# Performance work log

Measured on AMD Instinct MI355X. Metric: run time of the kernel, lower is better.

Reference implementation:

```python
import jax, jax.numpy as jnp
import numpy as np

BS, SL, D_IN, D_MODEL, H = 4, 128, 512, 512, 8
DP = D_MODEL // H


def setup_inputs() -> dict:
    key = jax.random.key(0)
    ks = jax.random.split(key, 12)
    s = 0.02
    inp = {
        "q": jax.random.normal(ks[0], (BS, SL, D_IN), jnp.float32),
        "k": jax.random.normal(ks[1], (BS, SL, D_IN), jnp.float32),
        "v": jax.random.normal(ks[2], (BS, SL, D_IN), jnp.float32),
    }
    j = jnp.arange(SL)
    # mask[t, jk] = 1.0 for the zero-padded slots jk > t in the shuffled sequence for step t
    mask2d = (j[None, :] > j[:, None]).astype(jnp.float32)  # (SL, SL)
    inp["mask"] = mask2d[None, :, None, None, :]            # (1, SL, 1, 1, SL)
    for i, n in enumerate(["wq", "wk", "wv", "dense"]):
        din = D_IN if n != "dense" else D_MODEL
        inp[n + "_w"] = jax.random.normal(ks[3 + 2 * i], (din, D_MODEL), jnp.float32) * s
        inp[n + "_b"] = jnp.zeros((D_MODEL,), jnp.float32)
    return inp


def _shuffle_idx(key, sl):
    # Row t of returned idx: random permutation of [0..t-1], then t, then t+1.. (padding slots).
    u = jax.random.uniform(key, (sl, sl))
    j = jnp.arange(sl)
    t = j[:, None]
    sort_keys = jnp.where(j[None, :] < t, u, j[None, :].astype(jnp.float32) + 2.0)
    return jnp.argsort(sort_keys, axis=-1)  # (sl, sl) int32


def _split_heads_shuffled(x, idx, valid):
    # x: (bs, sl, d) -> (bs, sl, H, sl, DP); padding slots (j > t) zeroed like torch plc_holder
    bs, sl, d = x.shape
    xt = x[:, idx, :] * valid[None, :, :, None]  # (bs, sl, sl, d)
    xt = xt.reshape(bs, sl, sl, H, DP)
    return xt.transpose(0, 1, 3, 2, 4)


def reference(q, k, v, mask, wq_w, wq_b, wk_w, wk_b, wv_w, wv_b, dense_w, dense_b):
    bs, sl, _ = q.shape
    j = jnp.arange(sl)
    valid = (j[None, :] <= j[:, None]).astype(q.dtype)  # (sl, sl)
    pkey = jax.random.key(42)
    idx_q = _shuffle_idx(jax.random.fold_in(pkey, 0), sl)
    idx_k = _shuffle_idx(jax.random.fold_in(pkey, 1), sl)
    idx_v = _shuffle_idx(jax.random.fold_in(pkey, 2), sl)

    qp = q @ wq_w + wq_b
    kp = k @ wk_w + wk_b
    vp = v @ wv_w + wv_b

    qh = _split_heads_shuffled(qp, idx_q, valid)  # (bs, sl, H, sl, DP)
    kh = _split_heads_shuffled(kp, idx_k, valid)
    vh = _split_heads_shuffled(vp, idx_v, valid)

    logits = jnp.einsum('bthqd,bthkd->bthqk', qh, kh) / jnp.sqrt(jnp.float32(DP))
    logits = logits + mask * (-1e9)
    attn = jax.nn.softmax(logits, axis=-1)          # (bs, sl, H, sl, sl)
    ctx = jnp.einsum('bthqk,bthkd->bthqd', attn, vh)  # (bs, sl, H, sl, DP)

    ctx = ctx.transpose(0, 1, 3, 2, 4).reshape(bs, sl, sl, H * DP)
    eff = ctx[:, j, j, :]                           # query row t of step t (the token itself)
    out = eff @ dense_w + dense_b                   # (bs, sl, d_model); dropout p=0 -> identity
    return (out, attn)
```

## Files before the change

### kernel.cpp

```cpp
#include <hip/hip_runtime.h>
#include <stdint.h>


#define BSZ 4
#define SLEN 128
#define DMODEL 512
#define NHEAD 8
#define HDIM 64

__device__ __forceinline__ uint32_t rotl32(uint32_t v, int d) {
  return (v << d) | (v >> (32 - d));
}

__device__ __forceinline__ void tf2x32(uint32_t k0, uint32_t k1, uint32_t x0,
                                       uint32_t x1, uint32_t& y0, uint32_t& y1) {
  uint32_t ks2 = k0 ^ k1 ^ 0x1BD11BDAu;
  x0 += k0; x1 += k1;
#define TF_R(r) { x0 += x1; x1 = rotl32(x1, (r)); x1 ^= x0; }
  TF_R(13) TF_R(15) TF_R(26) TF_R(6)
  x0 += k1;  x1 += ks2 + 1u;
  TF_R(17) TF_R(29) TF_R(16) TF_R(24)
  x0 += ks2; x1 += k0 + 2u;
  TF_R(13) TF_R(15) TF_R(26) TF_R(6)
  x0 += k0;  x1 += k1 + 3u;
  TF_R(17) TF_R(29) TF_R(16) TF_R(24)
  x0 += k1;  x1 += ks2 + 4u;
  TF_R(13) TF_R(15) TF_R(26) TF_R(6)
  x0 += ks2; x1 += k0 + 5u;
#undef TF_R
  y0 = x0; y1 = x1;
}

__global__ __launch_bounds__(128) void idx_kernel(int* __restrict__ idx) {
  const int m = blockIdx.x;
  const int t = blockIdx.y;
  const int j = threadIdx.x;
  __shared__ float u[SLEN];
  uint32_t fk0, fk1;
  tf2x32(0u, 42u, 0u, (uint32_t)m, fk0, fk1);
  const int flat = t * SLEN + j;
  uint32_t y0, y1;
  tf2x32(fk0, fk1, 0u, (uint32_t)flat, y0, y1);
  uint32_t bits = y0 ^ y1;
  float uu = __uint_as_float((bits >> 9) | 0x3f800000u) - 1.0f;
  u[j] = uu;
  __syncthreads();
  int* row = idx + (m * SLEN + t) * SLEN;
  if (j >= t) {
    row[j] = j;
  } else {
    int rank = 0;
    for (int i = 0; i < t; ++i) {
      float ui = u[i];
      rank += ((ui < uu) || (ui == uu && i < j)) ? 1 : 0;
    }
    row[rank] = j;
  }
}

__device__ __forceinline__ void gemm512_body(const float* __restrict__ A,
                                             const float* __restrict__ W,
                                             const float* __restrict__ bias,
                                             float* __restrict__ C,
                                             float* As , float* Ws ) {
  const int tid = threadIdx.x;
  const int tx = tid & 15, ty = tid >> 4;
  const int row0 = blockIdx.y * 64, col0 = blockIdx.x * 64;
  const int lr = tid >> 2, lc = (tid & 3) << 2;
  const int wr = tid >> 4, wc = (tid & 15) << 2;
  float acc[4][4] = {};
  for (int k0 = 0; k0 < 512; k0 += 16) {
    float4 av = *(const float4*)(A + (size_t)(row0 + lr) * 512 + k0 + lc);
    float4 wv = *(const float4*)(W + (size_t)(k0 + wr) * 512 + col0 + wc);
    As[lr * 17 + lc + 0] = av.x; As[lr * 17 + lc + 1] = av.y;
    As[lr * 17 + lc + 2] = av.z; As[lr * 17 + lc + 3] = av.w;
    *(float4*)(Ws + wr * 64 + wc) = wv;
    __syncthreads();
#pragma unroll
    for (int kk = 0; kk < 16; ++kk) {
      float a[4], b[4];
#pragma unroll
      for (int i = 0; i < 4; ++i) a[i] = As[(ty * 4 + i) * 17 + kk];
#pragma unroll
      for (int jj = 0; jj < 4; ++jj) b[jj] = Ws[kk * 64 + tx * 4 + jj];
#pragma unroll
      for (int i = 0; i < 4; ++i)
#pragma unroll
        for (int jj = 0; jj < 4; ++jj) acc[i][jj] += a[i] * b[jj];
    }
    __syncthreads();
  }
#pragma unroll
  for (int i = 0; i < 4; ++i) {
    int r = row0 + ty * 4 + i, c = col0 + tx * 4;
    float4 o;
    o.x = acc[i][0] + bias[c + 0];
    o.y = acc[i][1] + bias[c + 1];
    o.z = acc[i][2] + bias[c + 2];
    o.w = acc[i][3] + bias[c + 3];
    *(float4*)(C + (size_t)r * 512 + c) = o;
  }
}

__global__ __launch_bounds__(256) void proj_kernel(
    const float* __restrict__ q, const float* __restrict__ k, const float* __restrict__ v,
    const float* __restrict__ wq, const float* __restrict__ wk, const float* __restrict__ wv,
    const float* __restrict__ bq, const float* __restrict__ bk, const float* __restrict__ bv,
    float* __restrict__ qp, float* __restrict__ kp, float* __restrict__ vp) {
  __shared__ float As[64 * 17];
  __shared__ float Ws[16 * 64];
  const float* A; const float* W; const float* B; float* C;
  if (blockIdx.z == 0)      { A = q; W = wq; B = bq; C = qp; }
  else if (blockIdx.z == 1) { A = k; W = wk; B = bk; C = kp; }
  else                      { A = v; W = wv; B = bv; C = vp; }
  gemm512_body(A, W, B, C, As, Ws);
}

__global__ __launch_bounds__(256) void dense_kernel(const float* __restrict__ A,
                                                    const float* __restrict__ W,
                                                    const float* __restrict__ B,
                                                    float* __restrict__ C) {
  __shared__ float As[64 * 17];
  __shared__ float Ws[16 * 64];
  gemm512_body(A, W, B, C, As, Ws);
}

__global__ __launch_bounds__(256) void s_kernel(const float* __restrict__ qp,
                                                const float* __restrict__ kp,
                                                float* __restrict__ S) {
  const int h = blockIdx.x, b = blockIdx.y;
  const int tid = threadIdx.x;
  __shared__ float qs[SLEN * 33];
  __shared__ float ks[SLEN * 33];
  const float* qbase = qp + ((size_t)b * SLEN) * DMODEL + h * HDIM;
  const float* kbase = kp + ((size_t)b * SLEN) * DMODEL + h * HDIM;
  const int i0 = (tid >> 4) * 8, j0 = (tid & 15) * 8;
  float acc[8][8] = {};
  for (int d0 = 0; d0 < HDIM; d0 += 32) {
    __syncthreads();
    for (int it = 0; it < 4; ++it) {
      int flat = it * 256 + tid;
      int row = flat >> 3;
      int c4 = (flat & 7) << 2;
      float4 a = *(const float4*)(qbase + (size_t)row * DMODEL + d0 + c4);
      float4 bb = *(const float4*)(kbase + (size_t)row * DMODEL + d0 + c4);
      qs[row * 33 + c4 + 0] = a.x;  qs[row * 33 + c4 + 1] = a.y;
      qs[row * 33 + c4 + 2] = a.z;  qs[row * 33 + c4 + 3] = a.w;
      ks[row * 33 + c4 + 0] = bb.x; ks[row * 33 + c4 + 1] = bb.y;
      ks[row * 33 + c4 + 2] = bb.z; ks[row * 33 + c4 + 3] = bb.w;
    }
    __syncthreads();
    for (int d = 0; d < 32; ++d) {
      float a[8], bb[8];
#pragma unroll
      for (int r = 0; r < 8; ++r) a[r] = qs[(i0 + r) * 33 + d];
#pragma unroll
      for (int c = 0; c < 8; ++c) bb[c] = ks[(j0 + c) * 33 + d];
#pragma unroll
      for (int r = 0; r < 8; ++r)
#pragma unroll
        for (int c = 0; c < 8; ++c) acc[r][c] += a[r] * bb[c];
    }
  }
  float* Sb = S + (size_t)(b * NHEAD + h) * SLEN * SLEN;
#pragma unroll
  for (int r = 0; r < 8; ++r) {
    float4 o0, o1;
    o0.x = acc[r][0] * 0.125f; o0.y = acc[r][1] * 0.125f;
    o0.z = acc[r][2] * 0.125f; o0.w = acc[r][3] * 0.125f;
    o1.x = acc[r][4] * 0.125f; o1.y = acc[r][5] * 0.125f;
    o1.z = acc[r][6] * 0.125f; o1.w = acc[r][7] * 0.125f;
    *(float4*)(Sb + (size_t)(i0 + r) * SLEN + j0) = o0;
    *(float4*)(Sb + (size_t)(i0 + r) * SLEN + j0 + 4) = o1;
  }
}

__global__ __launch_bounds__(128) void ef_kernel(const float* __restrict__ S,
                                                 float* __restrict__ E,
                                                 float* __restrict__ Ft) {
  const int bh = blockIdx.x;
  const int i = threadIdx.x;
  __shared__ float m127s[SLEN];
  const float* Sb = S + (size_t)bh * SLEN * SLEN;
  const float* Srow = Sb + (size_t)i * SLEN;
  float m = -3.402823466e38f;
  for (int j = 0; j < SLEN; ++j) m = fmaxf(m, Srow[j]);
  m127s[i] = m;
  float rm = -3.402823466e38f, rl = 0.f;
  float* Fb = Ft + (size_t)bh * SLEN * SLEN;
  for (int t = 0; t < SLEN; ++t) {
    float sv = Srow[t];
    float nm = fmaxf(rm, sv);
    rl = rl * __expf(rm - nm) + __expf(sv - nm);
    rm = nm;
    Fb[t * SLEN + i] = __expf(m - nm) / rl;
  }
  __syncthreads();
  float* Eb = E + (size_t)bh * SLEN * SLEN;
  for (int flat = i; flat < SLEN * SLEN; flat += SLEN) {
    int r = flat >> 7;
    Eb[flat] = __expf(Sb[flat] - m127s[r]);
  }
}

__global__ __launch_bounds__(256) void attn_kernel(const float* __restrict__ E,
                                                   const float* __restrict__ Ft,
                                                   const int* __restrict__ idx,
                                                   const float* __restrict__ vp,
                                                   float* __restrict__ attn_out,
                                                   float* __restrict__ eff) {
  const int h = blockIdx.x, t = blockIdx.y, b = blockIdx.z;
  const int tid = threadIdx.x;
  const int wave = tid >> 6, lane = tid & 63;
  __shared__ int iqs[SLEN], iks[SLEN], ivs[SLEN];
  __shared__ float arow[SLEN];
  if (tid < SLEN) {
    iqs[tid] = idx[(0 * SLEN + t) * SLEN + tid];
    iks[tid] = idx[(1 * SLEN + t) * SLEN + tid];
    ivs[tid] = idx[(2 * SLEN + t) * SLEN + tid];
  }
  __syncthreads();
  const int bh = b * NHEAD + h;
  const float* Eb = E + (size_t)bh * SLEN * SLEN;
  const float* Fb = Ft + ((size_t)bh * SLEN + t) * SLEN;
  const float inv = 1.0f / (float)(t + 1);
  float* obase = attn_out + ((size_t)((b * SLEN + t) * NHEAD + h)) * SLEN * SLEN;
  const int k0 = lane * 2, k1 = lane * 2 + 1;
  for (int q = wave; q < SLEN; q += 4) {
    float2 val;
    if (q <= t) {
      int iq = iqs[q];
      float f = Fb[iq];
      const float* Er = Eb + (size_t)iq * SLEN;
      val.x = (k0 <= t) ? Er[iks[k0]] * f : 0.f;
      val.y = (k1 <= t) ? Er[iks[k1]] * f : 0.f;
    } else {
      val.x = (k0 <= t) ? inv : 0.f;
      val.y = (k1 <= t) ? inv : 0.f;
    }
    *(float2*)(obase + (size_t)q * SLEN + k0) = val;
    if (q == t) { arow[k0] = val.x; arow[k1] = val.y; }
  }
  __syncthreads();
  if (tid < HDIM) {
    const int d = tid;
    const float* vb = vp + (size_t)b * SLEN * DMODEL + h * HDIM + d;
    float acc = 0.f;
    for (int k = 0; k <= t; ++k) acc += arow[k] * vb[(size_t)ivs[k] * DMODEL];
    eff[((size_t)b * SLEN + t) * DMODEL + h * HDIM + d] = acc;
  }
}

extern "C" void kernel_launch(void* const* d_in, const int* in_sizes, int n_in,
                              void* d_out, int out_size, void* d_ws, size_t ws_size,
                              hipStream_t stream) {
  const float* q    = (const float*)d_in[0];
  const float* k    = (const float*)d_in[1];
  const float* v    = (const float*)d_in[2];
  const float* wq_w = (const float*)d_in[4];
  const float* wq_b = (const float*)d_in[5];
  const float* wk_w = (const float*)d_in[6];
  const float* wk_b = (const float*)d_in[7];
  const float* wv_w = (const float*)d_in[8];
  const float* wv_b = (const float*)d_in[9];
  const float* dw   = (const float*)d_in[10];
  const float* db   = (const float*)d_in[11];

  float* out  = (float*)d_out;
  float* attn = out + 262144;

  int*   idx = (int*)d_ws;
  float* wsf = (float*)d_ws;
  float* qp  = wsf + 49152;
  float* kp  = qp + 262144;
  float* vp  = kp + 262144;
  float* S   = vp + 262144;
  float* E   = S + 524288;
  float* Ft  = E + 524288;
  float* eff = Ft + 524288;
  (void)in_sizes; (void)n_in; (void)out_size; (void)ws_size;

  idx_kernel<<<dim3(3, 128, 1), 128, 0, stream>>>(idx);
  proj_kernel<<<dim3(8, 8, 3), 256, 0, stream>>>(q, k, v, wq_w, wk_w, wv_w,
                                                 wq_b, wk_b, wv_b, qp, kp, vp);
  s_kernel<<<dim3(8, 4, 1), 256, 0, stream>>>(qp, kp, S);
  ef_kernel<<<dim3(32, 1, 1), 128, 0, stream>>>(S, E, Ft);
  attn_kernel<<<dim3(8, 128, 4), 256, 0, stream>>>(E, Ft, idx, vp, attn, eff);
  dense_kernel<<<dim3(8, 8, 1), 256, 0, stream>>>(eff, dw, db, out);
}
```

Before: 439.6 us.

## Store exp table in bf16, stage it in LDS, retile GEMMs, split PV reduction

Stores the exponentiated score table E as bf16 instead of fp32. Each attention block copies the first t+1 rows of E for its (b,h) into shared memory and reads from there instead of doing scattered global gathers. The projection and dense GEMMs move to 128-thread blocks with 4x8 register tiles and transposed shared-memory layouts for float4 reads, and the score kernel uses the same transposed layout. The final attention-times-V product is split across all four waves with a shared-memory reduction. Rounding E to bf16 lowers the precision of the returned attention probabilities, and the 32KB shared buffer per block may reduce occupancy of attn_kernel.

```diff
diff --git a/kernel.cpp b/kernel.cpp
--- a/kernel.cpp
+++ b/kernel.cpp
@@ -31,6 +31,14 @@
   y0 = x0; y1 = x1;
 }
 
+__device__ __forceinline__ uint16_t f32_to_bf16(float v) {
+  uint32_t x = __float_as_uint(v);
+  return (uint16_t)((x + 0x7FFFu + ((x >> 16) & 1u)) >> 16);
+}
+__device__ __forceinline__ float bf16_to_f32(uint16_t b) {
+  return __uint_as_float(((uint32_t)b) << 16);
+}
+
 __global__ __launch_bounds__(128) void idx_kernel(int* __restrict__ idx) {
   const int m = blockIdx.x;
   const int t = blockIdx.y;
@@ -64,50 +72,56 @@
                                              float* __restrict__ C,
                                              float* As , float* Ws ) {
   const int tid = threadIdx.x;
-  const int tx = tid & 15, ty = tid >> 4;
+  const int tx = tid & 7, ty = tid >> 3;
   const int row0 = blockIdx.y * 64, col0 = blockIdx.x * 64;
-  const int lr = tid >> 2, lc = (tid & 3) << 2;
-  const int wr = tid >> 4, wc = (tid & 15) << 2;
-  float acc[4][4] = {};
+  const int ar = tid >> 1, ac = (tid & 1) * 8;
+  const int wr = tid >> 3, wc = (tid & 7) * 8;
+  float acc[4][8] = {};
   for (int k0 = 0; k0 < 512; k0 += 16) {
-    float4 av = *(const float4*)(A + (size_t)(row0 + lr) * 512 + k0 + lc);
-    float4 wv = *(const float4*)(W + (size_t)(k0 + wr) * 512 + col0 + wc);
-    As[lr * 17 + lc + 0] = av.x; As[lr * 17 + lc + 1] = av.y;
-    As[lr * 17 + lc + 2] = av.z; As[lr * 17 + lc + 3] = av.w;
-    *(float4*)(Ws + wr * 64 + wc) = wv;
+    float4 a0 = *(const float4*)(A + (size_t)(row0 + ar) * 512 + k0 + ac);
+    float4 a1 = *(const float4*)(A + (size_t)(row0 + ar) * 512 + k0 + ac + 4);
+    float4 w0 = *(const float4*)(W + (size_t)(k0 + wr) * 512 + col0 + wc);
+    float4 w1 = *(const float4*)(W + (size_t)(k0 + wr) * 512 + col0 + wc + 4);
+    As[(ac + 0) * 68 + ar] = a0.x; As[(ac + 1) * 68 + ar] = a0.y;
+    As[(ac + 2) * 68 + ar] = a0.z; As[(ac + 3) * 68 + ar] = a0.w;
+    As[(ac + 4) * 68 + ar] = a1.x; As[(ac + 5) * 68 + ar] = a1.y;
+    As[(ac + 6) * 68 + ar] = a1.z; As[(ac + 7) * 68 + ar] = a1.w;
+    *(float4*)(Ws + wr * 64 + wc) = w0;
+    *(float4*)(Ws + wr * 64 + wc + 4) = w1;
     __syncthreads();
 #pragma unroll
     for (int kk = 0; kk < 16; ++kk) {
-      float a[4], b[4];
-#pragma unroll
-      for (int i = 0; i < 4; ++i) a[i] = As[(ty * 4 + i) * 17 + kk];
-#pragma unroll
-      for (int jj = 0; jj < 4; ++jj) b[jj] = Ws[kk * 64 + tx * 4 + jj];
+      float4 a = *(const float4*)(As + kk * 68 + ty * 4);
+      float4 b0 = *(const float4*)(Ws + kk * 64 + tx * 8);
+      float4 b1 = *(const float4*)(Ws + kk * 64 + tx * 8 + 4);
+      float av[4] = {a.x, a.y, a.z, a.w};
+      float bv[8] = {b0.x, b0.y, b0.z, b0.w, b1.x, b1.y, b1.z, b1.w};
 #pragma unroll
       for (int i = 0; i < 4; ++i)
 #pragma unroll
-        for (int jj = 0; jj < 4; ++jj) acc[i][jj] += a[i] * b[jj];
+        for (int jj = 0; jj < 8; ++jj) acc[i][jj] += av[i] * bv[jj];
     }
     __syncthreads();
   }
 #pragma unroll
   for (int i = 0; i < 4; ++i) {
-    int r = row0 + ty * 4 + i, c = col0 + tx * 4;
-    float4 o;
-    o.x = acc[i][0] + bias[c + 0];
-    o.y = acc[i][1] + bias[c + 1];
-    o.z = acc[i][2] + bias[c + 2];
-    o.w = acc[i][3] + bias[c + 3];
-    *(float4*)(C + (size_t)r * 512 + c) = o;
-  }
-}
-
-__global__ __launch_bounds__(256) void proj_kernel(
+    int r = row0 + ty * 4 + i, c = col0 + tx * 8;
+    float4 o0, o1;
+    o0.x = acc[i][0] + bias[c + 0]; o0.y = acc[i][1] + bias[c + 1];
+    o0.z = acc[i][2] + bias[c + 2]; o0.w = acc[i][3] + bias[c + 3];
+    o1.x = acc[i][4] + bias[c + 4]; o1.y = acc[i][5] + bias[c + 5];
+    o1.z = acc[i][6] + bias[c + 6]; o1.w = acc[i][7] + bias[c + 7];
+    *(float4*)(C + (size_t)r * 512 + c) = o0;
+    *(float4*)(C + (size_t)r * 512 + c + 4) = o1;
+  }
+}
+
+__global__ __launch_bounds__(128) void proj_kernel(
     const float* __restrict__ q, const float* __restrict__ k, const float* __restrict__ v,
     const float* __restrict__ wq, const float* __restrict__ wk, const float* __restrict__ wv,
     const float* __restrict__ bq, const float* __restrict__ bk, const float* __restrict__ bv,
     float* __restrict__ qp, float* __restrict__ kp, float* __restrict__ vp) {
-  __shared__ float As[64 * 17];
+  __shared__ float As[16 * 68];
   __shared__ float Ws[16 * 64];
   const float* A; const float* W; const float* B; float* C;
   if (blockIdx.z == 0)      { A = q; W = wq; B = bq; C = qp; }
@@ -116,11 +130,11 @@
   gemm512_body(A, W, B, C, As, Ws);
 }
 
-__global__ __launch_bounds__(256) void dense_kernel(const float* __restrict__ A,
+__global__ __launch_bounds__(128) void dense_kernel(const float* __restrict__ A,
                                                     const float* __restrict__ W,
                                                     const float* __restrict__ B,
                                                     float* __restrict__ C) {
-  __shared__ float As[64 * 17];
+  __shared__ float As[16 * 68];
   __shared__ float Ws[16 * 64];
   gemm512_body(A, W, B, C, As, Ws);
 }
@@ -130,8 +144,8 @@
                                                 float* __restrict__ S) {
   const int h = blockIdx.x, b = blockIdx.y;
   const int tid = threadIdx.x;
-  __shared__ float qs[SLEN * 33];
-  __shared__ float ks[SLEN * 33];
+  __shared__ float qs[32 * 132];
+  __shared__ float ks[32 * 132];
   const float* qbase = qp + ((size_t)b * SLEN) * DMODEL + h * HDIM;
   const float* kbase = kp + ((size_t)b * SLEN) * DMODEL + h * HDIM;
   const int i0 = (tid >> 4) * 8, j0 = (tid & 15) * 8;
@@ -144,18 +158,19 @@
       int c4 = (flat & 7) << 2;
       float4 a = *(const float4*)(qbase + (size_t)row * DMODEL + d0 + c4);
       float4 bb = *(const float4*)(kbase + (size_t)row * DMODEL + d0 + c4);
-      qs[row * 33 + c4 + 0] = a.x;  qs[row * 33 + c4 + 1] = a.y;
-      qs[row * 33 + c4 + 2] = a.z;  qs[row * 33 + c4 + 3] = a.w;
-      ks[row * 33 + c4 + 0] = bb.x; ks[row * 33 + c4 + 1] = bb.y;
-      ks[row * 33 + c4 + 2] = bb.z; ks[row * 33 + c4 + 3] = bb.w;
+      qs[(c4 + 0) * 132 + row] = a.x;  qs[(c4 + 1) * 132 + row] = a.y;
+      qs[(c4 + 2) * 132 + row] = a.z;  qs[(c4 + 3) * 132 + row] = a.w;
+      ks[(c4 + 0) * 132 + row] = bb.x; ks[(c4 + 1) * 132 + row] = bb.y;
+      ks[(c4 + 2) * 132 + row] = bb.z; ks[(c4 + 3) * 132 + row] = bb.w;
     }
     __syncthreads();
     for (int d = 0; d < 32; ++d) {
-      float a[8], bb[8];
-#pragma unroll
-      for (int r = 0; r < 8; ++r) a[r] = qs[(i0 + r) * 33 + d];
-#pragma unroll
-      for (int c = 0; c < 8; ++c) bb[c] = ks[(j0 + c) * 33 + d];
+      float4 qa = *(const float4*)(qs + d * 132 + i0);
+      float4 qb = *(const float4*)(qs + d * 132 + i0 + 4);
+      float4 ka = *(const float4*)(ks + d * 132 + j0);
+      float4 kb = *(const float4*)(ks + d * 132 + j0 + 4);
+      float a[8] = {qa.x, qa.y, qa.z, qa.w, qb.x, qb.y, qb.z, qb.w};
+      float bb[8] = {ka.x, ka.y, ka.z, ka.w, kb.x, kb.y, kb.z, kb.w};
 #pragma unroll
       for (int r = 0; r < 8; ++r)
 #pragma unroll
@@ -176,7 +191,7 @@
 }
 
 __global__ __launch_bounds__(128) void ef_kernel(const float* __restrict__ S,
-                                                 float* __restrict__ E,
+                                                 uint16_t* __restrict__ E,
                                                  float* __restrict__ Ft) {
   const int bh = blockIdx.x;
   const int i = threadIdx.x;
@@ -196,14 +211,14 @@
     Fb[t * SLEN + i] = __expf(m - nm) / rl;
   }
   __syncthreads();
-  float* Eb = E + (size_t)bh * SLEN * SLEN;
+  uint16_t* Eb = E + (size_t)bh * SLEN * SLEN;
   for (int flat = i; flat < SLEN * SLEN; flat += SLEN) {
     int r = flat >> 7;
-    Eb[flat] = __expf(Sb[flat] - m127s[r]);
-  }
-}
-
-__global__ __launch_bounds__(256) void attn_kernel(const float* __restrict__ E,
+    Eb[flat] = f32_to_bf16(__expf(Sb[flat] - m127s[r]));
+  }
+}
+
+__global__ __launch_bounds__(256) void attn_kernel(const uint16_t* __restrict__ E,
                                                    const float* __restrict__ Ft,
                                                    const int* __restrict__ idx,
                                                    const float* __restrict__ vp,
@@ -212,42 +227,57 @@
   const int h = blockIdx.x, t = blockIdx.y, b = blockIdx.z;
   const int tid = threadIdx.x;
   const int wave = tid >> 6, lane = tid & 63;
+  __shared__ uint16_t Et[SLEN * SLEN];
   __shared__ int iqs[SLEN], iks[SLEN], ivs[SLEN];
+  __shared__ float Fs[SLEN];
   __shared__ float arow[SLEN];
+  __shared__ float red[256];
+  const int bh = b * NHEAD + h;
   if (tid < SLEN) {
     iqs[tid] = idx[(0 * SLEN + t) * SLEN + tid];
     iks[tid] = idx[(1 * SLEN + t) * SLEN + tid];
     ivs[tid] = idx[(2 * SLEN + t) * SLEN + tid];
-  }
-  __syncthreads();
-  const int bh = b * NHEAD + h;
-  const float* Eb = E + (size_t)bh * SLEN * SLEN;
-  const float* Fb = Ft + ((size_t)bh * SLEN + t) * SLEN;
+    Fs[tid] = Ft[((size_t)bh * SLEN + t) * SLEN + tid];
+  }
+  const uint16_t* Ebh = E + (size_t)bh * SLEN * SLEN;
+  const int nsh = (t + 1) * SLEN;
+  for (int off = tid * 4; off < nsh; off += 1024) {
+    *(ushort4*)(Et + off) = *(const ushort4*)(Ebh + off);
+  }
+  __syncthreads();
   const float inv = 1.0f / (float)(t + 1);
   float* obase = attn_out + ((size_t)((b * SLEN + t) * NHEAD + h)) * SLEN * SLEN;
-  const int k0 = lane * 2, k1 = lane * 2 + 1;
+  const int k0 = lane * 2, k1 = k0 + 1;
+  const int ik0 = iks[k0], ik1 = iks[k1];
+  const bool k0ok = (k0 <= t), k1ok = (k1 <= t);
   for (int q = wave; q < SLEN; q += 4) {
     float2 val;
     if (q <= t) {
       int iq = iqs[q];
-      float f = Fb[iq];
-      const float* Er = Eb + (size_t)iq * SLEN;
-      val.x = (k0 <= t) ? Er[iks[k0]] * f : 0.f;
-      val.y = (k1 <= t) ? Er[iks[k1]] * f : 0.f;
+      float f = Fs[iq];
+      float e0 = bf16_to_f32(Et[iq * SLEN + ik0]);
+      float e1 = bf16_to_f32(Et[iq * SLEN + ik1]);
+      val.x = k0ok ? e0 * f : 0.f;
+      val.y = k1ok ? e1 * f : 0.f;
     } else {
-      val.x = (k0 <= t) ? inv : 0.f;
-      val.y = (k1 <= t) ? inv : 0.f;
+      val.x = k0ok ? inv : 0.f;
+      val.y = k1ok ? inv : 0.f;
     }
     *(float2*)(obase + (size_t)q * SLEN + k0) = val;
     if (q == t) { arow[k0] = val.x; arow[k1] = val.y; }
   }
   __syncthreads();
-  if (tid < HDIM) {
-    const int d = tid;
+  {
+    const int d = tid & 63, kg = tid >> 6;
     const float* vb = vp + (size_t)b * SLEN * DMODEL + h * HDIM + d;
     float acc = 0.f;
-    for (int k = 0; k <= t; ++k) acc += arow[k] * vb[(size_t)ivs[k] * DMODEL];
-    eff[((size_t)b * SLEN + t) * DMODEL + h * HDIM + d] = acc;
+    for (int k = kg; k <= t; k += 4) acc += arow[k] * vb[(size_t)ivs[k] * DMODEL];
+    red[tid] = acc;
+  }
+  __syncthreads();
+  if (tid < HDIM) {
+    float r = red[tid] + red[tid + 64] + red[tid + 128] + red[tid + 192];
+    eff[((size_t)b * SLEN + t) * DMODEL + h * HDIM + tid] = r;
   }
 }
 
@@ -269,22 +299,22 @@
   float* out  = (float*)d_out;
   float* attn = out + 262144;
 
-  int*   idx = (int*)d_ws;
   float* wsf = (float*)d_ws;
-  float* qp  = wsf + 49152;
+  uint16_t* E = (uint16_t*)wsf;
+  int*   idx = (int*)(wsf + 262144);
+  float* qp  = wsf + 311296;
   float* kp  = qp + 262144;
   float* vp  = kp + 262144;
   float* S   = vp + 262144;
-  float* E   = S + 524288;
-  float* Ft  = E + 524288;
+  float* Ft  = S + 524288;
   float* eff = Ft + 524288;
   (void)in_sizes; (void)n_in; (void)out_size; (void)ws_size;
 
   idx_kernel<<<dim3(3, 128, 1), 128, 0, stream>>>(idx);
-  proj_kernel<<<dim3(8, 8, 3), 256, 0, stream>>>(q, k, v, wq_w, wk_w, wv_w,
+  proj_kernel<<<dim3(8, 8, 3), 128, 0, stream>>>(q, k, v, wq_w, wk_w, wv_w,
                                                  wq_b, wk_b, wv_b, qp, kp, vp);
   s_kernel<<<dim3(8, 4, 1), 256, 0, stream>>>(qp, kp, S);
   ef_kernel<<<dim3(32, 1, 1), 128, 0, stream>>>(S, E, Ft);
   attn_kernel<<<dim3(8, 128, 4), 256, 0, stream>>>(E, Ft, idx, vp, attn, eff);
-  dense_kernel<<<dim3(8, 8, 1), 256, 0, stream>>>(eff, dw, db, out);
-}
+  dense_kernel<<<dim3(8, 8, 1), 128, 0, stream>>>(eff, dw, db, out);
+}
```

Result: slower. 456.1 us (+3.7%).
